# Kernel tuning notes

Hardware: AMD Instinct MI355X
Metric: run time of the kernel (lower is better)

Reference implementation:

```python
import jax, jax.numpy as jnp
import numpy as np

N = 50000
NEG_SLOPE = 0.2


def leaky_relu(x, slope=NEG_SLOPE):
    return jnp.where(x >= 0, x, slope * x)


def gat_conv(x, edge_index, W, a_src, a_dst, bias):
    """PyG GATConv, heads=1, add_self_loops=True.
    x: [N, Fin], edge_index: [2, E] (row 0 = source j, row 1 = target i),
    W: [Fin, Fout], a_src/a_dst: [Fout], bias: [Fout].
    """
    n = x.shape[0]
    # add self loops
    loops = jnp.arange(n, dtype=edge_index.dtype)
    src = jnp.concatenate([edge_index[0], loops])
    dst = jnp.concatenate([edge_index[1], loops])

    xw = x @ W                       # [N, Fout]
    alpha_src = xw @ a_src           # [N]
    alpha_dst = xw @ a_dst           # [N]

    e = leaky_relu(alpha_src[src] + alpha_dst[dst])   # [E+N]
    # segment softmax over edges sharing the same target node
    m = jax.ops.segment_max(e, dst, num_segments=n)   # [N]
    ex = jnp.exp(e - m[dst])
    denom = jax.ops.segment_sum(ex, dst, num_segments=n)  # [N] (>0 via self loops)
    att = ex / denom[dst]                              # [E+N]

    msgs = att[:, None] * xw[src]                      # [E+N, Fout]
    out = jax.ops.segment_sum(msgs, dst, num_segments=n)
    return out + bias


def setup_inputs() -> dict:
    key = jax.random.key(0)
    ks = jax.random.split(key, 12)
    E = 800000
    Fin, H, Fout = 128, 256, 128
    x = jax.random.normal(ks[0], (N, Fin), dtype=jnp.float32)
    edge_index = jax.random.randint(ks[1], (2, E), 0, N, dtype=jnp.int64)
    s = 0.1
    W1 = jax.random.normal(ks[2], (Fin, H), dtype=jnp.float32) * s
    a1_src = jax.random.normal(ks[3], (H,), dtype=jnp.float32) * s
    a1_dst = jax.random.normal(ks[4], (H,), dtype=jnp.float32) * s
    b1 = jax.random.normal(ks[5], (H,), dtype=jnp.float32) * s
    W2 = jax.random.normal(ks[6], (H, Fout), dtype=jnp.float32) * s
    a2_src = jax.random.normal(ks[7], (Fout,), dtype=jnp.float32) * s
    a2_dst = jax.random.normal(ks[8], (Fout,), dtype=jnp.float32) * s
    b2 = jax.random.normal(ks[9], (Fout,), dtype=jnp.float32) * s
    return {"x": x, "edge_index": edge_index, "W1": W1, "a1_src": a1_src,
            "a1_dst": a1_dst, "b1": b1, "W2": W2, "a2_src": a2_src,
            "a2_dst": a2_dst, "b2": b2}


def reference(x, edge_index, W1, a1_src, a1_dst, b1, W2, a2_src, a2_dst, b2):
    h = jax.nn.relu(gat_conv(x, edge_index, W1, a1_src, a1_dst, b1))
    return gat_conv(h, edge_index, W2, a2_src, a2_dst, b2)
```

## Files before the change

### kernel.cpp

```cpp
#include <hip/hip_runtime.h>
#include <hip/hip_bf16.h>

typedef __attribute__((ext_vector_type(8))) short short8;
typedef __attribute__((ext_vector_type(4))) float floatx4;

#define CAP 8192
#define BIN_CH 2048

__device__ __forceinline__ float read_f(const void* p, long long i, int fp32m) {
  return fp32m ? ((const float*)p)[i] : (float)((const __hip_bfloat16*)p)[i];
}
__device__ __forceinline__ float bf2f(unsigned short u) {
  return __uint_as_float((unsigned)u << 16);
}
__device__ __forceinline__ unsigned short f2bf(float f) {
  const unsigned u = __float_as_uint(f);
  return (unsigned short)((u + 0x7fffu + ((u >> 16) & 1u)) >> 16);
}

__device__ __forceinline__ void pack_one(const void* W, unsigned short* Wp, int i,
                                         int K, int NOUT, int m) {
  const int k = i / NOUT, n = i - k * NOUT;
  const int ct = n >> 4, c = n & 15, ks = k >> 5, quad = (k >> 3) & 3, j = k & 7;
  Wp[(((ct * (K / 32) + ks) * 4 + quad) * 16 + c) * 8 + j] = f2bf(read_f(W, i, m));
}

__global__ __launch_bounds__(256) void prep_k(const void* __restrict__ x,
                                              const void* __restrict__ ei,
                                              const void* __restrict__ W1,
                                              const void* __restrict__ a1s,
                                              const void* __restrict__ a1d,
                                              const void* __restrict__ b1,
                                              const void* __restrict__ W2,
                                              const void* __restrict__ a2s,
                                              const void* __restrict__ a2d,
                                              const void* __restrict__ b2,
                                              unsigned short* __restrict__ Wp1,
                                              unsigned short* __restrict__ Wp2,
                                              float* __restrict__ w_as1, float* __restrict__ w_ad1,
                                              float* __restrict__ v_a2s, float* __restrict__ v_a2d,
                                              float* __restrict__ v_b1,  float* __restrict__ v_b2,
                                              int* __restrict__ bkcnt,
                                              int* __restrict__ flags) {
  __shared__ int fl_s[2];
  const int t = threadIdx.x, b = blockIdx.x;
  if (t < 64) {
    const unsigned short w = ((const unsigned short*)x)[t * 2];
    const int ef = (w >> 7) & 0xff;
    const bool bf_ok = (ef >= 90 && ef <= 140);
    const unsigned hi = ((const unsigned*)ei)[t * 2 + 1];
    const unsigned long long bm = __ballot(bf_ok);
    const unsigned long long zm = __ballot(hi == 0u);
    if (t == 0) {
      fl_s[0] = (bm == ~0ull) ? 0 : 1;
      fl_s[1] = (zm == ~0ull) ? 1 : 0;
      if (b == 0) { flags[0] = fl_s[0]; flags[1] = fl_s[1]; }
    }
  }
  __syncthreads();
  const int m = fl_s[0];

  if (b < 128) {
    pack_one(W1, Wp1, b * 256 + t, 128, 256, m);
  } else if (b < 256) {
    pack_one(W2, Wp2, (b - 128) * 256 + t, 256, 128, m);
  } else if (b == 256) {
    if (t < 128) {
      float sa = 0.f, sb = 0.f;
      for (int j = 0; j < 256; ++j) {
        const float w = read_f(W1, (long long)t * 256 + j, m);
        sa = fmaf(w, read_f(a1s, j, m), sa);
        sb = fmaf(w, read_f(a1d, j, m), sb);
      }
      w_as1[t] = sa;
      w_ad1[t] = sb;
    }
  } else if (b == 257) {
    if (t < 128) v_a2s[t] = read_f(a2s, t, m);
    else         v_a2d[t - 128] = read_f(a2d, t - 128, m);
  } else if (b == 258) {
    v_b1[t] = read_f(b1, t, m);
  } else {
    if (t < 128) v_b2[t] = read_f(b2, t, m);
    bkcnt[t] = 0;
  }
}

__global__ __launch_bounds__(256) void canon_alpha_k(const void* __restrict__ x,
                                                     const float* __restrict__ was,
                                                     const float* __restrict__ wad,
                                                     unsigned short* __restrict__ xb,
                                                     float* __restrict__ as_, float* __restrict__ ad_,
                                                     int n, const int* __restrict__ flags) {
  const int gid = blockIdx.x * 256 + threadIdx.x;
  const int node = gid >> 6, lane = gid & 63;
  if (node >= n) return;
  const int m = flags[0];
  const long long base = (long long)node * 128 + lane * 2;
  const float v0 = read_f(x, base, m), v1 = read_f(x, base + 1, m);
  ushort2 q;
  q.x = f2bf(v0); q.y = f2bf(v1);
  *(ushort2*)(xb + base) = q;
  float s1 = fmaf(v0, was[lane * 2], v1 * was[lane * 2 + 1]);
  float s2 = fmaf(v0, wad[lane * 2], v1 * wad[lane * 2 + 1]);
  for (int off = 32; off; off >>= 1) {
    s1 += __shfl_down(s1, off);
    s2 += __shfl_down(s2, off);
  }
  if (lane == 0) { as_[node] = s1; ad_[node] = s2; }
}

__device__ __forceinline__ void edge_sd(const void* ei, int e, int E, int i64m, int n,
                                        int& s, int& d) {
  if (e < E) {
    if (i64m) { s = (int)((const long long*)ei)[e]; d = (int)((const long long*)ei)[E + e]; }
    else      { s = ((const int*)ei)[e];            d = ((const int*)ei)[E + e]; }
  } else { s = d = e - E; }
  s = min(max(s, 0), n - 1);
  d = min(max(d, 0), n - 1);
}

__global__ __launch_bounds__(256) void bin_k(const void* __restrict__ ei,
                                             unsigned* __restrict__ bpool,
                                             int* __restrict__ bkcnt,
                                             int E, int EN, int n,
                                             const int* __restrict__ flags) {
  __shared__ unsigned stage[BIN_CH];
  __shared__ unsigned daddr[BIN_CH];
  __shared__ int bcnt_s[256], boff_s[256], gbase_s[256], sd[256];
  __shared__ int vtot_s;
  const int t = threadIdx.x;
  const int c0 = blockIdx.x * BIN_CH;
  const int i64m = flags[1];
  bcnt_s[t] = 0;
  __syncthreads();

  unsigned val[BIN_CH / 256];
  int buk[BIN_CH / 256];
#pragma unroll
  for (int i = 0; i < BIN_CH / 256; ++i) {
    const int e = c0 + i * 256 + t;
    if (e < EN) {
      int s, d;
      edge_sd(ei, e, E, i64m, n, s, d);
      buk[i] = d >> 8;
      val[i] = (unsigned)s | ((unsigned)(d & 255) << 16);
      atomicAdd(&bcnt_s[buk[i]], 1);
    } else buk[i] = -1;
  }
  __syncthreads();

  const int c = bcnt_s[t];
  sd[t] = c;
  __syncthreads();
  for (int off = 1; off < 256; off <<= 1) {
    const int v = (t >= off) ? sd[t - off] : 0;
    __syncthreads();
    sd[t] += v;
    __syncthreads();
  }
  boff_s[t] = sd[t] - c;
  if (t == 255) vtot_s = sd[255];
  gbase_s[t] = (c > 0) ? atomicAdd(&bkcnt[t], c) : 0;
  bcnt_s[t] = 0;
  __syncthreads();

#pragma unroll
  for (int i = 0; i < BIN_CH / 256; ++i) {
    if (buk[i] >= 0) {
      const int lp = atomicAdd(&bcnt_s[buk[i]], 1);
      const int si = boff_s[buk[i]] + lp;
      stage[si] = val[i];
      const int gp = gbase_s[buk[i]] + lp;
      daddr[si] = (gp < CAP) ? (unsigned)(buk[i] * CAP + gp) : 0xFFFFFFFFu;
    }
  }
  __syncthreads();

  const int vt = vtot_s;
  for (int idx = t; idx < vt; idx += 256)
    if (daddr[idx] != 0xFFFFFFFFu) bpool[daddr[idx]] = stage[idx];
}

__global__ __launch_bounds__(256) void bucket_csr_k(const unsigned* __restrict__ bpool,
                                                    const int* __restrict__ bkcnt,
                                                    unsigned short* __restrict__ csrc,
                                                    int* __restrict__ start_g,
                                                    int* __restrict__ deg_g, int n) {
  __shared__ int deg_s[256], cur_s[256], sd[256];
  const int t = threadIdx.x, b = blockIdx.x;
  int cnt = bkcnt[b];
  if (cnt > CAP) cnt = CAP;
  deg_s[t] = 0;
  __syncthreads();
  for (int idx = t; idx < cnt; idx += 256) {
    const unsigned v = bpool[b * CAP + idx];
    atomicAdd(&deg_s[(v >> 16) & 255], 1);
  }
  __syncthreads();
  const int dg = deg_s[t];
  sd[t] = dg;
  __syncthreads();
  for (int off = 1; off < 256; off <<= 1) {
    const int v = (t >= off) ? sd[t - off] : 0;
    __syncthreads();
    sd[t] += v;
    __syncthreads();
  }
  const int excl = sd[t] - dg;
  const int node = b * 256 + t;
  if (node < n) { start_g[node] = b * CAP + excl; deg_g[node] = dg; }
  cur_s[t] = excl;
  __syncthreads();
  for (int idx = t; idx < cnt; idx += 256) {
    const unsigned v = bpool[b * CAP + idx];
    const int p = atomicAdd(&cur_s[(v >> 16) & 255], 1);
    csrc[b * CAP + p] = (unsigned short)(v & 0xFFFFu);
  }
}

template<int K, int NOUT, bool HID>
__global__ __launch_bounds__(256) void gemm_mfma_k(const unsigned short* __restrict__ A,
                                                   const unsigned short* __restrict__ Wp,
                                                   unsigned short* __restrict__ outp,
                                                   const float* __restrict__ bias,
                                                   const float* __restrict__ av_src,
                                                   const float* __restrict__ av_dst,
                                                   float* __restrict__ as_, float* __restrict__ ad_,
                                                   int nrows) {
  constexpr int KS = K / 32;
  constexpr int CT = NOUT / 16;
  const int wave = threadIdx.x >> 6, lane = threadIdx.x & 63;
  const int quad = lane >> 4, c = lane & 15;
  const int row0 = (blockIdx.x * 4 + wave) * 16;
  if (row0 >= nrows) return;
  int arow = row0 + c;
  if (arow >= nrows) arow = nrows - 1;

  short8 afrag[KS];
  const unsigned short* Ab = A + (size_t)arow * K;
#pragma unroll
  for (int ks = 0; ks < KS; ++ks)
    afrag[ks] = *(const short8*)(Ab + ks * 32 + quad * 8);

  float pa_s[4] = {0.f, 0.f, 0.f, 0.f}, pa_d[4] = {0.f, 0.f, 0.f, 0.f};
#pragma unroll
  for (int ct = 0; ct < CT; ++ct) {
    floatx4 acc = {0.f, 0.f, 0.f, 0.f};
#pragma unroll
    for (int ks = 0; ks < KS; ++ks) {
      const short8 bfrag = *(const short8*)(Wp + (size_t)((ct * KS + ks) * 64 + lane) * 8);
      acc = __builtin_amdgcn_mfma_f32_16x16x32_bf16(afrag[ks], bfrag, acc, 0, 0, 0);
    }
    if constexpr (HID) {
      const float bv = bias[ct * 16 + c];
#pragma unroll
      for (int r = 0; r < 4; ++r) {
        const int rr = row0 + quad * 4 + r;
        const float v = acc[r] + bv;
        if (rr < nrows) outp[(size_t)rr * NOUT + ct * 16 + c] = f2bf(v > 0.f ? v : 0.f);
      }
    } else {
      const float asv = av_src[ct * 16 + c], adv = av_dst[ct * 16 + c];
#pragma unroll
      for (int r = 0; r < 4; ++r) {
        const int rr = row0 + quad * 4 + r;
        pa_s[r] = fmaf(acc[r], asv, pa_s[r]);
        pa_d[r] = fmaf(acc[r], adv, pa_d[r]);
        if (rr < nrows) outp[(size_t)rr * NOUT + ct * 16 + c] = f2bf(acc[r]);
      }
    }
  }
  if constexpr (!HID) {
    for (int off = 1; off < 16; off <<= 1) {
#pragma unroll
      for (int r = 0; r < 4; ++r) {
        pa_s[r] += __shfl_xor(pa_s[r], off);
        pa_d[r] += __shfl_xor(pa_d[r], off);
      }
    }
    if (c == 0) {
#pragma unroll
      for (int r = 0; r < 4; ++r) {
        const int rr = row0 + quad * 4 + r;
        if (rr < nrows) { as_[rr] = pa_s[r]; ad_[rr] = pa_d[r]; }
      }
    }
  }
}

template<int MODE>
__global__ __launch_bounds__(256) void agg_csr_k(const int* __restrict__ start_g,
                                                 const int* __restrict__ deg_g,
                                                 const unsigned short* __restrict__ csrc,
                                                 const float* __restrict__ as_,
                                                 const float* __restrict__ ad_,
                                                 const unsigned short* __restrict__ xw,
                                                 const float* __restrict__ bias,
                                                 void* __restrict__ outp, int n,
                                                 const int* __restrict__ flags) {
  const int gid = blockIdx.x * 256 + threadIdx.x;
  const int node = gid >> 6, lane = gid & 63;
  if (node >= n) return;
  const int start = start_g[node], end = start + deg_g[node];
  const float adv = ad_[node];
  const int slot = lane >> 4;
  const int col  = lane & 15;

  float acc[8] = {0.f, 0.f, 0.f, 0.f, 0.f, 0.f, 0.f, 0.f};
  float dsum = 0.f;

  for (int base = start; base < end; base += 64) {
    const int idx = base + lane;
    int s_pre = 0;
    float w_pre = 0.f;
    if (idx < end) {
      s_pre = (int)csrc[idx];
      float v = as_[s_pre] + adv;
      v = (v >= 0.f) ? v : 0.2f * v;
      w_pre = __expf(fminf(v, 60.f));
    }
    dsum += w_pre;
    const int cnt = min(64, end - base);
    for (int j = 0; j < cnt; j += 8) {
      const int jj0 = j + slot, jj1 = j + 4 + slot;
      int s0 = __shfl(s_pre, jj0);
      float w0 = __shfl(w_pre, jj0);
      int s1 = __shfl(s_pre, jj1);
      float w1 = __shfl(w_pre, jj1);
      const bool ok0 = (jj0 < cnt), ok1 = (jj1 < cnt);
      s0 = ok0 ? s0 : 0; w0 = ok0 ? w0 : 0.f;
      s1 = ok1 ? s1 : 0; w1 = ok1 ? w1 : 0.f;
      const short8 q0 = *(const short8*)(xw + (size_t)s0 * 128 + col * 8);
      const short8 q1 = *(const short8*)(xw + (size_t)s1 * 128 + col * 8);
#pragma unroll
      for (int c = 0; c < 8; ++c) {
        acc[c] = fmaf(w0, bf2f((unsigned short)q0[c]), acc[c]);
        acc[c] = fmaf(w1, bf2f((unsigned short)q1[c]), acc[c]);
      }
    }
  }

  for (int off = 32; off; off >>= 1) dsum += __shfl_down(dsum, off);
  dsum = __shfl(dsum, 0);
  const float r = 1.f / fmaxf(dsum, 1e-30f);

#pragma unroll
  for (int c = 0; c < 8; ++c) {
    acc[c] += __shfl_xor(acc[c], 16);
    acc[c] += __shfl_xor(acc[c], 32);
  }

  if (slot == 0) {
    const int c0 = col * 8;
    if constexpr (MODE == 0) {
      short8 q;
#pragma unroll
      for (int c = 0; c < 8; ++c) q[c] = (short)f2bf(acc[c] * r);
      *(short8*)((unsigned short*)outp + (size_t)node * 128 + c0) = q;
    } else {
      if (flags[0]) {
        float* o = (float*)outp + (size_t)node * 128 + c0;
        floatx4 q0, q1;
#pragma unroll
        for (int c = 0; c < 4; ++c) {
          q0[c] = fmaf(acc[c], r, bias[c0 + c]);
          q1[c] = fmaf(acc[c + 4], r, bias[c0 + 4 + c]);
        }
        *(floatx4*)o = q0;
        *(floatx4*)(o + 4) = q1;
      } else {
        short8 q;
#pragma unroll
        for (int c = 0; c < 8; ++c) q[c] = (short)f2bf(fmaf(acc[c], r, bias[c0 + c]));
        *(short8*)((unsigned short*)outp + (size_t)node * 128 + c0) = q;
      }
    }
  }
}

extern "C" void kernel_launch(void* const* d_in, const int* in_sizes, int n_in,
                              void* d_out, int out_size, void* d_ws, size_t ws_size,
                              hipStream_t stream) {
  const void* x   = d_in[0];
  const void* ei  = d_in[1];
  const void* W1  = d_in[2];
  const void* a1s = d_in[3];
  const void* a1d = d_in[4];
  const void* b1  = d_in[5];
  const void* W2  = d_in[6];
  const void* a2s = d_in[7];
  const void* a2d = d_in[8];
  const void* b2  = d_in[9];

  const int N  = in_sizes[0] / 128;
  const int E  = in_sizes[1] / 2;
  const int EN = E + N;
  const int NBUK = (N + 255) / 256;

  unsigned short* B1 = (unsigned short*)d_ws;
  unsigned short* B2 = B1 + (size_t)N * 128;
  unsigned short* H  = B2 + (size_t)N * 128;
  float* as_   = (float*)(H + (size_t)N * 256);
  float* ad_   = as_ + N;
  int*   start_g = (int*)(ad_ + N);
  int*   deg_g   = start_g + N;
  int*   bkcnt   = deg_g + N;
  unsigned* bpool = (unsigned*)(bkcnt + 256);
  unsigned short* csrc = (unsigned short*)(bpool + (size_t)NBUK * CAP);
  unsigned short* Wp1 = csrc + (size_t)NBUK * CAP;
  unsigned short* Wp2 = Wp1 + 128 * 256;
  float* vecs  = (float*)(Wp2 + 256 * 128);
  int*   flags = (int*)(vecs + 1152);
  float* w_as1 = vecs,        *w_ad1 = vecs + 128;
  float* v_a2s = vecs + 256,  *v_a2d = vecs + 384;
  float* v_b1  = vecs + 512,  *v_b2  = vecs + 768;

  const int NB = (N * 64 + 255) / 256;
  const int BB = (EN + BIN_CH - 1) / BIN_CH;
  const int MB = (N + 63) / 64;

  prep_k<<<260, 256, 0, stream>>>(x, ei, W1, a1s, a1d, b1, W2, a2s, a2d, b2,
                                  Wp1, Wp2, w_as1, w_ad1, v_a2s, v_a2d, v_b1, v_b2,
                                  bkcnt, flags);

  canon_alpha_k<<<NB, 256, 0, stream>>>(x, w_as1, w_ad1, B1, as_, ad_, N, flags);

  bin_k<<<BB, 256, 0, stream>>>(ei, bpool, bkcnt, E, EN, N, flags);
  bucket_csr_k<<<NBUK, 256, 0, stream>>>(bpool, bkcnt, csrc, start_g, deg_g, N);

  agg_csr_k<0><<<NB, 256, 0, stream>>>(start_g, deg_g, csrc, as_, ad_, B1, nullptr, B2, N, flags);
  gemm_mfma_k<128, 256, true><<<MB, 256, 0, stream>>>(B2, Wp1, H, v_b1,
                                                      nullptr, nullptr, nullptr, nullptr, N);

  gemm_mfma_k<256, 128, false><<<MB, 256, 0, stream>>>(H, Wp2, B1, nullptr,
                                                       v_a2s, v_a2d, as_, ad_, N);
  agg_csr_k<1><<<NB, 256, 0, stream>>>(start_g, deg_g, csrc, as_, ad_, B1, v_b2, d_out, N, flags);
}
```

Baseline: 269.0 us.

## Fuse layer-1 aggregation with first GEMM via LDS staging

Merges the layer-1 neighbour aggregation and the hidden-layer MFMA GEMM into one kernel. Each 1024-thread block aggregates 16 nodes (one wave per node), stages the bf16 results in LDS, then each of the 16 waves computes one 16-column tile of the 256-wide hidden output. This removes the intermediate B2 buffer round trip through global memory and one kernel launch. In exchange it adds a block-wide barrier after the irregular aggregation, so waves on low-degree nodes sit idle until the highest-degree node in the block finishes, and large blocks may reduce scheduling flexibility.

```diff
diff --git a/kernel.cpp b/kernel.cpp
--- a/kernel.cpp
+++ b/kernel.cpp
@@ -219,96 +219,15 @@
   }
 }
 
-template<int K, int NOUT, bool HID>
-__global__ __launch_bounds__(256) void gemm_mfma_k(const unsigned short* __restrict__ A,
-                                                   const unsigned short* __restrict__ Wp,
-                                                   unsigned short* __restrict__ outp,
-                                                   const float* __restrict__ bias,
-                                                   const float* __restrict__ av_src,
-                                                   const float* __restrict__ av_dst,
-                                                   float* __restrict__ as_, float* __restrict__ ad_,
-                                                   int nrows) {
-  constexpr int KS = K / 32;
-  constexpr int CT = NOUT / 16;
-  const int wave = threadIdx.x >> 6, lane = threadIdx.x & 63;
-  const int quad = lane >> 4, c = lane & 15;
-  const int row0 = (blockIdx.x * 4 + wave) * 16;
-  if (row0 >= nrows) return;
-  int arow = row0 + c;
-  if (arow >= nrows) arow = nrows - 1;
-
-  short8 afrag[KS];
-  const unsigned short* Ab = A + (size_t)arow * K;
-#pragma unroll
-  for (int ks = 0; ks < KS; ++ks)
-    afrag[ks] = *(const short8*)(Ab + ks * 32 + quad * 8);
-
-  float pa_s[4] = {0.f, 0.f, 0.f, 0.f}, pa_d[4] = {0.f, 0.f, 0.f, 0.f};
-#pragma unroll
-  for (int ct = 0; ct < CT; ++ct) {
-    floatx4 acc = {0.f, 0.f, 0.f, 0.f};
-#pragma unroll
-    for (int ks = 0; ks < KS; ++ks) {
-      const short8 bfrag = *(const short8*)(Wp + (size_t)((ct * KS + ks) * 64 + lane) * 8);
-      acc = __builtin_amdgcn_mfma_f32_16x16x32_bf16(afrag[ks], bfrag, acc, 0, 0, 0);
-    }
-    if constexpr (HID) {
-      const float bv = bias[ct * 16 + c];
-#pragma unroll
-      for (int r = 0; r < 4; ++r) {
-        const int rr = row0 + quad * 4 + r;
-        const float v = acc[r] + bv;
-        if (rr < nrows) outp[(size_t)rr * NOUT + ct * 16 + c] = f2bf(v > 0.f ? v : 0.f);
-      }
-    } else {
-      const float asv = av_src[ct * 16 + c], adv = av_dst[ct * 16 + c];
-#pragma unroll
-      for (int r = 0; r < 4; ++r) {
-        const int rr = row0 + quad * 4 + r;
-        pa_s[r] = fmaf(acc[r], asv, pa_s[r]);
-        pa_d[r] = fmaf(acc[r], adv, pa_d[r]);
-        if (rr < nrows) outp[(size_t)rr * NOUT + ct * 16 + c] = f2bf(acc[r]);
-      }
-    }
-  }
-  if constexpr (!HID) {
-    for (int off = 1; off < 16; off <<= 1) {
-#pragma unroll
-      for (int r = 0; r < 4; ++r) {
-        pa_s[r] += __shfl_xor(pa_s[r], off);
-        pa_d[r] += __shfl_xor(pa_d[r], off);
-      }
-    }
-    if (c == 0) {
-#pragma unroll
-      for (int r = 0; r < 4; ++r) {
-        const int rr = row0 + quad * 4 + r;
-        if (rr < nrows) { as_[rr] = pa_s[r]; ad_[rr] = pa_d[r]; }
-      }
-    }
-  }
-}
-
-template<int MODE>
-__global__ __launch_bounds__(256) void agg_csr_k(const int* __restrict__ start_g,
-                                                 const int* __restrict__ deg_g,
-                                                 const unsigned short* __restrict__ csrc,
-                                                 const float* __restrict__ as_,
-                                                 const float* __restrict__ ad_,
-                                                 const unsigned short* __restrict__ xw,
-                                                 const float* __restrict__ bias,
-                                                 void* __restrict__ outp, int n,
-                                                 const int* __restrict__ flags) {
-  const int gid = blockIdx.x * 256 + threadIdx.x;
-  const int node = gid >> 6, lane = gid & 63;
-  if (node >= n) return;
-  const int start = start_g[node], end = start + deg_g[node];
-  const float adv = ad_[node];
-  const int slot = lane >> 4;
-  const int col  = lane & 15;
-
-  float acc[8] = {0.f, 0.f, 0.f, 0.f, 0.f, 0.f, 0.f, 0.f};
+__device__ __forceinline__ void agg_node(const int start, const int end,
+                                         const unsigned short* __restrict__ csrc,
+                                         const float* __restrict__ as_, const float adv,
+                                         const unsigned short* __restrict__ xw,
+                                         const int lane, float* acc) {
+  const int slot = lane >> 4, col = lane & 15;
   float dsum = 0.f;
+#pragma unroll
+  for (int c = 0; c < 8; ++c) acc[c] = 0.f;
 
   for (int base = start; base < end; base += 64) {
     const int idx = base + lane;
@@ -340,41 +259,156 @@
       }
     }
   }
-
   for (int off = 32; off; off >>= 1) dsum += __shfl_down(dsum, off);
   dsum = __shfl(dsum, 0);
   const float r = 1.f / fmaxf(dsum, 1e-30f);
-
 #pragma unroll
   for (int c = 0; c < 8; ++c) {
     acc[c] += __shfl_xor(acc[c], 16);
     acc[c] += __shfl_xor(acc[c], 32);
-  }
-
+    acc[c] *= r;
+  }
+}
+
+#define LSTR 136
+__global__ __launch_bounds__(1024) void agg_gemm1_k(const int* __restrict__ start_g,
+                                                    const int* __restrict__ deg_g,
+                                                    const unsigned short* __restrict__ csrc,
+                                                    const float* __restrict__ as_,
+                                                    const float* __restrict__ ad_,
+                                                    const unsigned short* __restrict__ xb,
+                                                    const unsigned short* __restrict__ Wp1,
+                                                    const float* __restrict__ v_b1,
+                                                    unsigned short* __restrict__ H, int n) {
+  __shared__ unsigned short lds[16 * LSTR];
+  const int wv = threadIdx.x >> 6, lane = threadIdx.x & 63;
+  const int slot = lane >> 4, col = lane & 15;
+  const int node = blockIdx.x * 16 + wv;
+
+  float acc[8];
+  if (node < n) {
+    const int start = start_g[node];
+    agg_node(start, start + deg_g[node], csrc, as_, ad_[node], xb, lane, acc);
+  } else {
+#pragma unroll
+    for (int c = 0; c < 8; ++c) acc[c] = 0.f;
+  }
+  if (slot == 0) {
+    short8 q;
+#pragma unroll
+    for (int c = 0; c < 8; ++c) q[c] = (short)f2bf(acc[c]);
+    *(short8*)&lds[wv * LSTR + col * 8] = q;
+  }
+  __syncthreads();
+
+  const int quad = slot, c = col;
+  floatx4 g = {0.f, 0.f, 0.f, 0.f};
+#pragma unroll
+  for (int ks = 0; ks < 4; ++ks) {
+    const short8 af = *(const short8*)&lds[c * LSTR + ks * 32 + quad * 8];
+    const short8 bf = *(const short8*)(Wp1 + (size_t)((wv * 4 + ks) * 64 + lane) * 8);
+    g = __builtin_amdgcn_mfma_f32_16x16x32_bf16(af, bf, g, 0, 0, 0);
+  }
+  const float bv = v_b1[wv * 16 + c];
+  const int row0 = blockIdx.x * 16;
+#pragma unroll
+  for (int r = 0; r < 4; ++r) {
+    const int rr = row0 + quad * 4 + r;
+    const float v = g[r] + bv;
+    if (rr < n) H[(size_t)rr * 256 + wv * 16 + c] = f2bf(v > 0.f ? v : 0.f);
+  }
+}
+
+template<int K, int NOUT>
+__global__ __launch_bounds__(256) void gemm_mfma_k(const unsigned short* __restrict__ A,
+                                                   const unsigned short* __restrict__ Wp,
+                                                   unsigned short* __restrict__ outp,
+                                                   const float* __restrict__ av_src,
+                                                   const float* __restrict__ av_dst,
+                                                   float* __restrict__ as_, float* __restrict__ ad_,
+                                                   int nrows) {
+  constexpr int KS = K / 32;
+  constexpr int CT = NOUT / 16;
+  const int wave = threadIdx.x >> 6, lane = threadIdx.x & 63;
+  const int quad = lane >> 4, c = lane & 15;
+  const int row0 = (blockIdx.x * 4 + wave) * 16;
+  if (row0 >= nrows) return;
+  int arow = row0 + c;
+  if (arow >= nrows) arow = nrows - 1;
+
+  short8 afrag[KS];
+  const unsigned short* Ab = A + (size_t)arow * K;
+#pragma unroll
+  for (int ks = 0; ks < KS; ++ks)
+    afrag[ks] = *(const short8*)(Ab + ks * 32 + quad * 8);
+
+  float pa_s[4] = {0.f, 0.f, 0.f, 0.f}, pa_d[4] = {0.f, 0.f, 0.f, 0.f};
+#pragma unroll
+  for (int ct = 0; ct < CT; ++ct) {
+    floatx4 acc = {0.f, 0.f, 0.f, 0.f};
+#pragma unroll
+    for (int ks = 0; ks < KS; ++ks) {
+      const short8 bfrag = *(const short8*)(Wp + (size_t)((ct * KS + ks) * 64 + lane) * 8);
+      acc = __builtin_amdgcn_mfma_f32_16x16x32_bf16(afrag[ks], bfrag, acc, 0, 0, 0);
+    }
+    const float asv = av_src[ct * 16 + c], adv = av_dst[ct * 16 + c];
+#pragma unroll
+    for (int r = 0; r < 4; ++r) {
+      const int rr = row0 + quad * 4 + r;
+      pa_s[r] = fmaf(acc[r], asv, pa_s[r]);
+      pa_d[r] = fmaf(acc[r], adv, pa_d[r]);
+      if (rr < nrows) outp[(size_t)rr * NOUT + ct * 16 + c] = f2bf(acc[r]);
+    }
+  }
+  for (int off = 1; off < 16; off <<= 1) {
+#pragma unroll
+    for (int r = 0; r < 4; ++r) {
+      pa_s[r] += __shfl_xor(pa_s[r], off);
+      pa_d[r] += __shfl_xor(pa_d[r], off);
+    }
+  }
+  if (c == 0) {
+#pragma unroll
+    for (int r = 0; r < 4; ++r) {
+      const int rr = row0 + quad * 4 + r;
+      if (rr < nrows) { as_[rr] = pa_s[r]; ad_[rr] = pa_d[r]; }
+    }
+  }
+}
+
+__global__ __launch_bounds__(256) void agg_out_k(const int* __restrict__ start_g,
+                                                 const int* __restrict__ deg_g,
+                                                 const unsigned short* __restrict__ csrc,
+                                                 const float* __restrict__ as_,
+                                                 const float* __restrict__ ad_,
+                                                 const unsigned short* __restrict__ xw,
+                                                 const float* __restrict__ bias,
+                                                 void* __restrict__ outp, int n,
+                                                 const int* __restrict__ flags) {
+  const int gid = blockIdx.x * 256 + threadIdx.x;
+  const int node = gid >> 6, lane = gid & 63;
+  if (node >= n) return;
+  const int slot = lane >> 4, col = lane & 15;
+  const int start = start_g[node];
+  float acc[8];
+  agg_node(start, start + deg_g[node], csrc, as_, ad_[node], xw, lane, acc);
   if (slot == 0) {
     const int c0 = col * 8;
-    if constexpr (MODE == 0) {
+    if (flags[0]) {
+      float* o = (float*)outp + (size_t)node * 128 + c0;
+      floatx4 q0, q1;
+#pragma unroll
+      for (int c = 0; c < 4; ++c) {
+        q0[c] = acc[c] + bias[c0 + c];
+        q1[c] = acc[c + 4] + bias[c0 + 4 + c];
+      }
+      *(floatx4*)o = q0;
+      *(floatx4*)(o + 4) = q1;
+    } else {
       short8 q;
 #pragma unroll
-      for (int c = 0; c < 8; ++c) q[c] = (short)f2bf(acc[c] * r);
+      for (int c = 0; c < 8; ++c) q[c] = (short)f2bf(acc[c] + bias[c0 + c]);
       *(short8*)((unsigned short*)outp + (size_t)node * 128 + c0) = q;
-    } else {
-      if (flags[0]) {
-        float* o = (float*)outp + (size_t)node * 128 + c0;
-        floatx4 q0, q1;
-#pragma unroll
-        for (int c = 0; c < 4; ++c) {
-          q0[c] = fmaf(acc[c], r, bias[c0 + c]);
-          q1[c] = fmaf(acc[c + 4], r, bias[c0 + 4 + c]);
-        }
-        *(floatx4*)o = q0;
-        *(floatx4*)(o + 4) = q1;
-      } else {
-        short8 q;
-#pragma unroll
-        for (int c = 0; c < 8; ++c) q[c] = (short)f2bf(fmaf(acc[c], r, bias[c0 + c]));
-        *(short8*)((unsigned short*)outp + (size_t)node * 128 + c0) = q;
-      }
     }
   }
 }
@@ -399,8 +433,7 @@
   const int NBUK = (N + 255) / 256;
 
   unsigned short* B1 = (unsigned short*)d_ws;
-  unsigned short* B2 = B1 + (size_t)N * 128;
-  unsigned short* H  = B2 + (size_t)N * 128;
+  unsigned short* H  = B1 + (size_t)N * 128;
   float* as_   = (float*)(H + (size_t)N * 256);
   float* ad_   = as_ + N;
   int*   start_g = (int*)(ad_ + N);
@@ -419,6 +452,7 @@
   const int NB = (N * 64 + 255) / 256;
   const int BB = (EN + BIN_CH - 1) / BIN_CH;
   const int MB = (N + 63) / 64;
+  const int AG = (N + 15) / 16;
 
   prep_k<<<260, 256, 0, stream>>>(x, ei, W1, a1s, a1d, b1, W2, a2s, a2d, b2,
                                   Wp1, Wp2, w_as1, w_ad1, v_a2s, v_a2d, v_b1, v_b2,
@@ -429,11 +463,8 @@
   bin_k<<<BB, 256, 0, stream>>>(ei, bpool, bkcnt, E, EN, N, flags);
   bucket_csr_k<<<NBUK, 256, 0, stream>>>(bpool, bkcnt, csrc, start_g, deg_g, N);
 
-  agg_csr_k<0><<<NB, 256, 0, stream>>>(start_g, deg_g, csrc, as_, ad_, B1, nullptr, B2, N, flags);
-  gemm_mfma_k<128, 256, true><<<MB, 256, 0, stream>>>(B2, Wp1, H, v_b1,
-                                                      nullptr, nullptr, nullptr, nullptr, N);
-
-  gemm_mfma_k<256, 128, false><<<MB, 256, 0, stream>>>(H, Wp2, B1, nullptr,
-                                                       v_a2s, v_a2d, as_, ad_, N);
-  agg_csr_k<1><<<NB, 256, 0, stream>>>(start_g, deg_g, csrc, as_, ad_, B1, v_b2, d_out, N, flags);
-}
+  agg_gemm1_k<<<AG, 1024, 0, stream>>>(start_g, deg_g, csrc, as_, ad_, B1, Wp1, v_b1, H, N);
+
+  gemm_mfma_k<256, 128><<<MB, 256, 0, stream>>>(H, Wp2, B1, v_a2s, v_a2d, as_, ad_, N);
+  agg_out_k<<<NB, 256, 0, stream>>>(start_g, deg_g, csrc, as_, ad_, B1, v_b2, d_out, N, flags);
+}
```

Result: faster. 262.5 us (-2.4%).
